# Optimization experiments

Hardware: AMD Instinct MI355X
Metric: run time of the kernel (lower is better)

The kernel has to match this reference:

```python
import jax, jax.numpy as jnp
import numpy as np

EPS = 1e-12


def _phi(e):
    # e: [C, L] -> pairwise euclidean distances [C, C], diagonal zeroed
    sq = jnp.sum(e * e, axis=1)                      # [C]
    prod = e @ e.T                                   # [C, C]
    d2 = sq[:, None] + sq[None, :] - 2.0 * prod
    d = jnp.sqrt(jnp.clip(d2, EPS, None))
    C = e.shape[0]
    return d * (1.0 - jnp.eye(C, dtype=e.dtype))


def setup_inputs() -> dict:
    key = jax.random.key(0)
    k1, k2, k3 = jax.random.split(key, 3)
    N, C, L = 64, 512, 256
    le_student = jax.random.normal(k1, (N, C, L), dtype=jnp.float32)
    le_teacher = jax.random.normal(k2, (N, C, L), dtype=jnp.float32)
    targets = jax.random.randint(k3, (N, C), 0, 2, dtype=jnp.int32)
    return {"le_student": le_student, "le_teacher": le_teacher, "targets": targets}


def reference(le_student, le_teacher, targets):
    N, C, L = le_student.shape
    m = targets.astype(le_student.dtype)             # [N, C] 0/1 mask
    es = le_student * m[:, :, None]                  # zero out negative rows
    et = le_teacher * m[:, :, None]

    Ds = jax.vmap(_phi)(es)                          # [N, C, C]
    Dt = jax.vmap(_phi)(et)                          # [N, C, C]

    eye = jnp.eye(C, dtype=m.dtype)
    pm = m[:, :, None] * m[:, None, :]               # pairs of positive rows
    offdiag = pm * (1.0 - eye)                       # off-diagonal positive pairs

    npos = jnp.sum(m, axis=1)                        # [N]
    cnt = npos * (npos - 1.0)                        # entries with d > 0 in submatrix
    valid = npos > 1.0
    safe_cnt = jnp.maximum(cnt, 1.0)

    mean_s = jnp.sum(Ds * offdiag, axis=(1, 2)) / safe_cnt
    mean_t = jax.lax.stop_gradient(jnp.sum(Dt * offdiag, axis=(1, 2)) / safe_cnt)
    mean_s = jnp.where(valid, mean_s, 1.0)
    mean_t = jnp.where(valid, mean_t, 1.0)

    d = Ds / mean_s[:, None, None]
    td = jax.lax.stop_gradient(Dt / mean_t[:, None, None])

    diff = d - td
    adiff = jnp.abs(diff)
    huber = jnp.where(adiff < 1.0, 0.5 * diff * diff, adiff - 0.5)

    per = jnp.sum(huber * pm, axis=(1, 2)) / jnp.maximum(npos, 1.0)
    return jnp.sum(jnp.where(valid, per, 0.0))
```

## Files before the change

kernel.cpp:

```cpp
#include <hip/hip_runtime.h>
#include <hip/hip_bf16.h>
#include <hip/hip_fp16.h>
#include <math.h>

#define NB 64
#define CC 512
#define LL 256

typedef __attribute__((ext_vector_type(4))) float floatx4;
typedef __attribute__((ext_vector_type(8))) short short8;

static __device__ __forceinline__ unsigned f2bf2(float x, float y) {
    __hip_bfloat162 h = __float22bfloat162_rn(make_float2(x, y));
    union { __hip_bfloat162 h; unsigned u; } c; c.h = h;
    return c.u;
}
static __device__ __forceinline__ unsigned short f2h(float x) {
    __half h = __float2half_rn(x);
    union { __half h; unsigned short u; } c; c.h = h;
    return c.u;
}
static __device__ __forceinline__ float h2f(unsigned u) {
    union { unsigned short u; __half h; } c; c.u = (unsigned short)u;
    return __half2float(c.h);
}

static __device__ __forceinline__ bool decode_tile(int t, int u, int& tI, int& tJ) {
    if (t >= (u * (u + 1)) >> 1) return false;
    tI = 0;
    while (t >= u - tI) { t -= u - tI; ++tI; }
    tJ = tI + t;
    return true;
}

__global__ __launch_bounds__(256) void dist_kernel(
    const float* __restrict__ S, const float* __restrict__ T,
    const int* __restrict__ targets,
    float* __restrict__ sumS, float* __restrict__ sumT,
    unsigned short* __restrict__ Ds, unsigned short* __restrict__ Dt,
    float* __restrict__ out)
{
    const int bx = blockIdx.x;
    const int n = bx & (NB - 1);
    const int q = bx >> 6;
    const int mat = q & 1, t = q >> 1;
    const int tid = threadIdx.x;
    const int w = tid >> 6, lane = tid & 63;

    __shared__ __align__(16) unsigned short lds[2][2][64][40];
    __shared__ float s_norm[2][64];
    __shared__ float red[4];
    __shared__ int s_idx[CC];
    __shared__ int s_cnt[8], s_off[8];
    __shared__ int s_np;

    if (bx == 0 && tid == 0) out[0] = 0.0f;

    const int* tg = targets + n * CC;
    const bool p0 = tg[tid] != 0;
    const bool p1 = tg[tid + 256] != 0;
    const unsigned long long m0 = __ballot(p0);
    const unsigned long long m1 = __ballot(p1);
    if (lane == 0) { s_cnt[w] = __popcll(m0); s_cnt[4 + w] = __popcll(m1); }
    __syncthreads();
    if (tid == 0) {
        int a = 0;
        for (int i = 0; i < 8; ++i) { s_off[i] = a; a += s_cnt[i]; }
        s_np = a;
    }
    __syncthreads();
    const unsigned long long below = (1ull << lane) - 1ull;
    if (p0) s_idx[s_off[w] + __popcll(m0 & below)] = tid;
    if (p1) s_idx[s_off[4 + w] + __popcll(m1 & below)] = tid + 256;
    const int np = s_np;
    __syncthreads();

    if (np < 2) return;
    int tI, tJ;
    if (!decode_tile(t, (np + 63) >> 6, tI, tJ)) return;
    const bool diag = (tI == tJ);

    const float* P = (mat ? T : S) + (size_t)n * CC * LL;
    unsigned short* Dout = (mat ? Dt : Ds) + (((size_t)t * NB + n) << 12);

    const int srow = w * 32 + (lane >> 1);
    const int half = lane & 1;
    const bool stager = diag ? (srow < 64) : true;
    const int ab = srow >> 6, rloc = srow & 63;
    const int gk = (ab ? tJ : tI) * 64 + rloc;
    const int row = s_idx[(gk < np) ? gk : 0];
    const char* rp = (const char*)P + (size_t)row * (LL * 4) + half * 64;

    float4 pre[4];
    float nsum = 0.0f;
    if (stager) {
        #pragma unroll
        for (int i = 0; i < 4; ++i) pre[i] = *(const float4*)(rp + i * 16);
    }

    const int m16 = lane & 15, quad = lane >> 4;
    const int bufB = diag ? 0 : 1;
    const int wrow = w * 16;

    floatx4 acc[4];
    #pragma unroll
    for (int c = 0; c < 4; ++c) { acc[c][0] = 0; acc[c][1] = 0; acc[c][2] = 0; acc[c][3] = 0; }

    for (int kk = 0; kk < 8; ++kk) {
        const int pb = kk & 1;
        if (stager) {
            #pragma unroll
            for (int i = 0; i < 4; ++i)
                nsum += pre[i].x * pre[i].x + pre[i].y * pre[i].y +
                        pre[i].z * pre[i].z + pre[i].w * pre[i].w;
            unsigned short* dst = &lds[ab][pb][rloc][half * 16];
            *(uint2*)(dst + 0)  = make_uint2(f2bf2(pre[0].x, pre[0].y), f2bf2(pre[0].z, pre[0].w));
            *(uint2*)(dst + 4)  = make_uint2(f2bf2(pre[1].x, pre[1].y), f2bf2(pre[1].z, pre[1].w));
            *(uint2*)(dst + 8)  = make_uint2(f2bf2(pre[2].x, pre[2].y), f2bf2(pre[2].z, pre[2].w));
            *(uint2*)(dst + 12) = make_uint2(f2bf2(pre[3].x, pre[3].y), f2bf2(pre[3].z, pre[3].w));
        }
        __syncthreads();
        if (stager && kk < 7) {
            #pragma unroll
            for (int i = 0; i < 4; ++i)
                pre[i] = *(const float4*)(rp + (kk + 1) * 128 + i * 16);
        }
        const short8 a = *(const short8*)&lds[0][pb][wrow + m16][quad * 8];
        #pragma unroll
        for (int c = 0; c < 4; ++c) {
            const short8 b = *(const short8*)&lds[bufB][pb][c * 16 + m16][quad * 8];
            acc[c] = __builtin_amdgcn_mfma_f32_16x16x32_bf16(a, b, acc[c], 0, 0, 0);
        }
    }

    if (stager) {
        const float v = nsum + __shfl_xor(nsum, 1);
        if (half == 0) s_norm[ab][rloc] = v;
    }
    __syncthreads();

    float l0 = 0.0f;
    #pragma unroll
    for (int c = 0; c < 4; ++c) {
        const int colL = c * 16 + m16;
        const int gj = tJ * 64 + colL;
        const float nB = s_norm[bufB][colL];
        #pragma unroll
        for (int r = 0; r < 4; ++r) {
            const int rowL = wrow + quad * 4 + r;
            const int gi = tI * 64 + rowL;
            const float d = sqrtf(fmaxf(s_norm[0][rowL] + nB - 2.0f * acc[c][r], 1e-12f));
            if (gi < np && gj < np && gi != gj) l0 += d;
            Dout[rowL * 64 + colL] = f2h(d);
        }
    }

    #pragma unroll
    for (int o = 32; o; o >>= 1) l0 += __shfl_down(l0, o);
    if (lane == 0) red[w] = l0;
    __syncthreads();
    if (tid == 0) {
        const float wgt = diag ? 1.0f : 2.0f;
        (mat ? sumT : sumS)[t * NB + n] = wgt * (red[0] + red[1] + red[2] + red[3]);
    }
}

__global__ __launch_bounds__(256) void huber_kernel(
    const int* __restrict__ targets,
    const float* __restrict__ sumS, const float* __restrict__ sumT,
    const unsigned short* __restrict__ Ds, const unsigned short* __restrict__ Dt,
    float* __restrict__ out)
{
    const int bx = blockIdx.x;
    const int n = bx & (NB - 1), t = bx >> 6;
    const int tid = threadIdx.x;
    const int w = tid >> 6, lane = tid & 63;

    __shared__ int s_cnt[8];
    __shared__ float red[4];

    const int* tg = targets + n * CC;
    const unsigned long long m0 = __ballot(tg[tid] != 0);
    const unsigned long long m1 = __ballot(tg[tid + 256] != 0);
    if (lane == 0) { s_cnt[w] = __popcll(m0); s_cnt[4 + w] = __popcll(m1); }
    __syncthreads();
    int np = 0;
    #pragma unroll
    for (int i = 0; i < 8; ++i) np += s_cnt[i];

    if (np < 2) return;
    const int u = (np + 63) >> 6;
    int tI, tJ;
    if (!decode_tile(t, u, tI, tJ)) return;
    const int ntiles = (u * (u + 1)) >> 1;

    float a = 0.0f, b = 0.0f;
    if (lane < ntiles) { a = sumS[lane * NB + n]; b = sumT[lane * NB + n]; }
    #pragma unroll
    for (int o = 32; o; o >>= 1) { a += __shfl_down(a, o); b += __shfl_down(b, o); }
    a = __shfl(a, 0); b = __shfl(b, 0);

    const float cnt = (float)np * (float)(np - 1);
    const float inv_ms = cnt / a;
    const float inv_mt = cnt / b;

    const size_t slot = ((size_t)t * NB + n) << 12;
    const uint4* ps = (const uint4*)(Ds + slot);
    const uint4* pt = (const uint4*)(Dt + slot);

    float h = 0.0f;
    #pragma unroll
    for (int it = 0; it < 2; ++it) {
        const int g = it * 256 + tid;
        const uint4 va = ps[g];
        const uint4 vb = pt[g];
        const unsigned aw[4] = { va.x, va.y, va.z, va.w };
        const unsigned bw[4] = { vb.x, vb.y, vb.z, vb.w };
        const int e0 = g * 8;
        #pragma unroll
        for (int k = 0; k < 8; ++k) {
            const int e = e0 + k;
            const int gi = tI * 64 + (e >> 6);
            const int gj = tJ * 64 + (e & 63);
            if (gi < np && gj < np && gi != gj) {
                const unsigned wa = aw[k >> 1], wb = bw[k >> 1];
                const float ds = h2f((k & 1) ? (wa >> 16) : (wa & 0xffffu));
                const float dt = h2f((k & 1) ? (wb >> 16) : (wb & 0xffffu));
                const float diff = ds * inv_ms - dt * inv_mt;
                const float ad = fabsf(diff);
                h += (ad < 1.0f) ? 0.5f * diff * diff : ad - 0.5f;
            }
        }
    }

    #pragma unroll
    for (int o = 32; o; o >>= 1) h += __shfl_down(h, o);
    if (lane == 0) red[w] = h;
    __syncthreads();
    if (tid == 0) {
        const float wgt = (tI == tJ) ? 1.0f : 2.0f;
        atomicAdd(out, wgt * (red[0] + red[1] + red[2] + red[3]) / (float)np);
    }
}

extern "C" void kernel_launch(void* const* d_in, const int* in_sizes, int n_in,
                              void* d_out, int out_size, void* d_ws, size_t ws_size,
                              hipStream_t stream) {
    const float* S = (const float*)d_in[0];
    const float* T = (const float*)d_in[1];
    const int* targets = (const int*)d_in[2];
    float* out = (float*)d_out;

    char* p = (char*)d_ws;
    float* sumS = (float*)p;   p += (size_t)36 * NB * 4;
    float* sumT = (float*)p;   p += (size_t)36 * NB * 4;
    p = (char*)(((size_t)p + 255) & ~(size_t)255);
    unsigned short* Ds = (unsigned short*)p;   p += (size_t)36 * NB * 4096 * 2;
    unsigned short* Dt = (unsigned short*)p;

    dist_kernel<<<72 * NB, 256, 0, stream>>>(S, T, targets, sumS, sumT, Ds, Dt, out);
    huber_kernel<<<36 * NB, 256, 0, stream>>>(targets, sumS, sumT, Ds, Dt, out);
}
```

Before: 122.2 us.

## Add pack kernel that compacts positive rows to bf16 with precomputed norms

```diff
diff --git a/kernel.cpp b/kernel.cpp
--- a/kernel.cpp
+++ b/kernel.cpp
@@ -33,28 +33,23 @@
     return true;
 }
 
-__global__ __launch_bounds__(256) void dist_kernel(
+__global__ __launch_bounds__(256) void pack_kernel(
     const float* __restrict__ S, const float* __restrict__ T,
     const int* __restrict__ targets,
-    float* __restrict__ sumS, float* __restrict__ sumT,
-    unsigned short* __restrict__ Ds, unsigned short* __restrict__ Dt,
+    int* __restrict__ npos, float* __restrict__ norms,
+    unsigned short* __restrict__ Sc, unsigned short* __restrict__ Tc,
     float* __restrict__ out)
 {
     const int bx = blockIdx.x;
     const int n = bx & (NB - 1);
     const int q = bx >> 6;
-    const int mat = q & 1, t = q >> 1;
+    const int mat = q & 1, slice = q >> 1;
     const int tid = threadIdx.x;
     const int w = tid >> 6, lane = tid & 63;
 
-    __shared__ __align__(16) unsigned short lds[2][2][64][40];
-    __shared__ float s_norm[2][64];
-    __shared__ float red[4];
     __shared__ int s_idx[CC];
     __shared__ int s_cnt[8], s_off[8];
     __shared__ int s_np;
-
-    if (bx == 0 && tid == 0) out[0] = 0.0f;
 
     const int* tg = targets + n * CC;
     const bool p0 = tg[tid] != 0;
@@ -67,6 +62,8 @@
         int a = 0;
         for (int i = 0; i < 8; ++i) { s_off[i] = a; a += s_cnt[i]; }
         s_np = a;
+        if (mat == 0 && slice == 0) npos[n] = a;
+        if (bx == 0) out[0] = 0.0f;
     }
     __syncthreads();
     const unsigned long long below = (1ull << lane) - 1ull;
@@ -75,28 +72,77 @@
     const int np = s_np;
     __syncthreads();
 
+    const int r = slice * 32 + (tid >> 3);
+    const int sub = tid & 7;
+    if (r >= np) return;
+    const int src = s_idx[r];
+    const float* P = (mat ? T : S) + ((size_t)n * CC + src) * LL + sub * 32;
+    unsigned short* Q = (mat ? Tc : Sc) + ((size_t)n * CC + r) * LL + sub * 32;
+
+    float4 v[8];
+    #pragma unroll
+    for (int i = 0; i < 8; ++i) v[i] = *(const float4*)(P + i * 4);
+    float ns = 0.0f;
+    #pragma unroll
+    for (int i = 0; i < 8; ++i)
+        ns += v[i].x * v[i].x + v[i].y * v[i].y + v[i].z * v[i].z + v[i].w * v[i].w;
+    ns += __shfl_xor(ns, 1); ns += __shfl_xor(ns, 2); ns += __shfl_xor(ns, 4);
+    if (sub == 0) norms[((size_t)mat * NB + n) * CC + r] = ns;
+
+    uint2 o[8];
+    #pragma unroll
+    for (int i = 0; i < 8; ++i) o[i] = make_uint2(f2bf2(v[i].x, v[i].y), f2bf2(v[i].z, v[i].w));
+    *(uint4*)(Q + 0)  = make_uint4(o[0].x, o[0].y, o[1].x, o[1].y);
+    *(uint4*)(Q + 8)  = make_uint4(o[2].x, o[2].y, o[3].x, o[3].y);
+    *(uint4*)(Q + 16) = make_uint4(o[4].x, o[4].y, o[5].x, o[5].y);
+    *(uint4*)(Q + 24) = make_uint4(o[6].x, o[6].y, o[7].x, o[7].y);
+}
+
+__global__ __launch_bounds__(256) void dist_kernel(
+    const unsigned short* __restrict__ Sc, const unsigned short* __restrict__ Tc,
+    const int* __restrict__ npos, const float* __restrict__ norms,
+    float* __restrict__ sumS, float* __restrict__ sumT,
+    unsigned short* __restrict__ Ds, unsigned short* __restrict__ Dt)
+{
+    const int bx = blockIdx.x;
+    const int n = bx & (NB - 1);
+    const int q = bx >> 6;
+    const int mat = q & 1, t = q >> 1;
+    const int np = npos[n];
     if (np < 2) return;
     int tI, tJ;
     if (!decode_tile(t, (np + 63) >> 6, tI, tJ)) return;
     const bool diag = (tI == tJ);
 
-    const float* P = (mat ? T : S) + (size_t)n * CC * LL;
+    __shared__ __align__(16) unsigned short lds[2][2][64][40];
+    __shared__ float s_norm[2][64];
+    __shared__ float red[4];
+
+    const int tid = threadIdx.x;
+    const int w = tid >> 6, lane = tid & 63;
+
+    const unsigned short* Pc = (mat ? Tc : Sc) + (size_t)n * CC * LL;
+    const float* nr = norms + ((size_t)mat * NB + n) * CC;
     unsigned short* Dout = (mat ? Dt : Ds) + (((size_t)t * NB + n) << 12);
+
+    if (tid < 128) {
+        const int abn = tid >> 6, rn = tid & 63;
+        if (!diag || abn == 0) {
+            const int g = (abn ? tJ : tI) * 64 + rn;
+            s_norm[abn][rn] = nr[(g < np) ? g : (np - 1)];
+        }
+    }
 
     const int srow = w * 32 + (lane >> 1);
     const int half = lane & 1;
     const bool stager = diag ? (srow < 64) : true;
     const int ab = srow >> 6, rloc = srow & 63;
     const int gk = (ab ? tJ : tI) * 64 + rloc;
-    const int row = s_idx[(gk < np) ? gk : 0];
-    const char* rp = (const char*)P + (size_t)row * (LL * 4) + half * 64;
-
-    float4 pre[4];
-    float nsum = 0.0f;
-    if (stager) {
-        #pragma unroll
-        for (int i = 0; i < 4; ++i) pre[i] = *(const float4*)(rp + i * 16);
-    }
+    const int crow = (gk < np) ? gk : (np - 1);
+    const unsigned char* rp = (const unsigned char*)(Pc + (size_t)crow * LL) + half * 32;
+
+    uint4 pre0, pre1;
+    if (stager) { pre0 = *(const uint4*)rp; pre1 = *(const uint4*)(rp + 16); }
 
     const int m16 = lane & 15, quad = lane >> 4;
     const int bufB = diag ? 0 : 1;
@@ -109,21 +155,14 @@
     for (int kk = 0; kk < 8; ++kk) {
         const int pb = kk & 1;
         if (stager) {
-            #pragma unroll
-            for (int i = 0; i < 4; ++i)
-                nsum += pre[i].x * pre[i].x + pre[i].y * pre[i].y +
-                        pre[i].z * pre[i].z + pre[i].w * pre[i].w;
             unsigned short* dst = &lds[ab][pb][rloc][half * 16];
-            *(uint2*)(dst + 0)  = make_uint2(f2bf2(pre[0].x, pre[0].y), f2bf2(pre[0].z, pre[0].w));
-            *(uint2*)(dst + 4)  = make_uint2(f2bf2(pre[1].x, pre[1].y), f2bf2(pre[1].z, pre[1].w));
-            *(uint2*)(dst + 8)  = make_uint2(f2bf2(pre[2].x, pre[2].y), f2bf2(pre[2].z, pre[2].w));
-            *(uint2*)(dst + 12) = make_uint2(f2bf2(pre[3].x, pre[3].y), f2bf2(pre[3].z, pre[3].w));
+            *(uint4*)(dst + 0) = pre0;
+            *(uint4*)(dst + 8) = pre1;
         }
         __syncthreads();
         if (stager && kk < 7) {
-            #pragma unroll
-            for (int i = 0; i < 4; ++i)
-                pre[i] = *(const float4*)(rp + (kk + 1) * 128 + i * 16);
+            pre0 = *(const uint4*)(rp + (kk + 1) * 64);
+            pre1 = *(const uint4*)(rp + (kk + 1) * 64 + 16);
         }
         const short8 a = *(const short8*)&lds[0][pb][wrow + m16][quad * 8];
         #pragma unroll
@@ -132,12 +171,6 @@
             acc[c] = __builtin_amdgcn_mfma_f32_16x16x32_bf16(a, b, acc[c], 0, 0, 0);
         }
     }
-
-    if (stager) {
-        const float v = nsum + __shfl_xor(nsum, 1);
-        if (half == 0) s_norm[ab][rloc] = v;
-    }
-    __syncthreads();
 
     float l0 = 0.0f;
     #pragma unroll
@@ -166,33 +199,23 @@
 }
 
 __global__ __launch_bounds__(256) void huber_kernel(
-    const int* __restrict__ targets,
+    const int* __restrict__ npos,
     const float* __restrict__ sumS, const float* __restrict__ sumT,
     const unsigned short* __restrict__ Ds, const unsigned short* __restrict__ Dt,
     float* __restrict__ out)
 {
     const int bx = blockIdx.x;
     const int n = bx & (NB - 1), t = bx >> 6;
-    const int tid = threadIdx.x;
-    const int w = tid >> 6, lane = tid & 63;
-
-    __shared__ int s_cnt[8];
-    __shared__ float red[4];
-
-    const int* tg = targets + n * CC;
-    const unsigned long long m0 = __ballot(tg[tid] != 0);
-    const unsigned long long m1 = __ballot(tg[tid + 256] != 0);
-    if (lane == 0) { s_cnt[w] = __popcll(m0); s_cnt[4 + w] = __popcll(m1); }
-    __syncthreads();
-    int np = 0;
-    #pragma unroll
-    for (int i = 0; i < 8; ++i) np += s_cnt[i];
-
+    const int np = npos[n];
     if (np < 2) return;
     const int u = (np + 63) >> 6;
     int tI, tJ;
     if (!decode_tile(t, u, tI, tJ)) return;
     const int ntiles = (u * (u + 1)) >> 1;
+
+    const int tid = threadIdx.x;
+    const int w = tid >> 6, lane = tid & 63;
+    __shared__ float red[4];
 
     float a = 0.0f, b = 0.0f;
     if (lane < ntiles) { a = sumS[lane * NB + n]; b = sumT[lane * NB + n]; }
@@ -252,12 +275,17 @@
     float* out = (float*)d_out;
 
     char* p = (char*)d_ws;
+    int* npos = (int*)p;       p += 256;
+    float* norms = (float*)p;  p += (size_t)2 * NB * CC * 4;
     float* sumS = (float*)p;   p += (size_t)36 * NB * 4;
     float* sumT = (float*)p;   p += (size_t)36 * NB * 4;
     p = (char*)(((size_t)p + 255) & ~(size_t)255);
-    unsigned short* Ds = (unsigned short*)p;   p += (size_t)36 * NB * 4096 * 2;
+    unsigned short* Sc = (unsigned short*)p;  p += (size_t)NB * CC * LL * 2;
+    unsigned short* Tc = (unsigned short*)p;  p += (size_t)NB * CC * LL * 2;
+    unsigned short* Ds = (unsigned short*)p;  p += (size_t)36 * NB * 4096 * 2;
     unsigned short* Dt = (unsigned short*)p;
 
-    dist_kernel<<<72 * NB, 256, 0, stream>>>(S, T, targets, sumS, sumT, Ds, Dt, out);
-    huber_kernel<<<36 * NB, 256, 0, stream>>>(targets, sumS, sumT, Ds, Dt, out);
-}
+    pack_kernel<<<32 * NB, 256, 0, stream>>>(S, T, targets, npos, norms, Sc, Tc, out);
+    dist_kernel<<<72 * NB, 256, 0, stream>>>(Sc, Tc, npos, norms, sumS, sumT, Ds, Dt);
+    huber_kernel<<<36 * NB, 256, 0, stream>>>(npos, sumS, sumT, Ds, Dt, out);
+}
```

Measured after the change: 129.2 us. 1.06x slower.

## Fuse distance and Huber kernels using last-block-done atomic counters

Applied to the files above, without the earlier changes.

```diff
diff --git a/kernel.cpp b/kernel.cpp
--- a/kernel.cpp
+++ b/kernel.cpp
@@ -23,6 +23,12 @@
 static __device__ __forceinline__ float h2f(unsigned u) {
     union { unsigned short u; __half h; } c; c.u = (unsigned short)u;
     return __half2float(c.h);
+}
+static __device__ __forceinline__ float ld_agent_f32(const float* p) {
+    return __hip_atomic_load(p, __ATOMIC_RELAXED, __HIP_MEMORY_SCOPE_AGENT);
+}
+static __device__ __forceinline__ unsigned long long ld_agent_u64(const unsigned long long* p) {
+    return __hip_atomic_load(p, __ATOMIC_RELAXED, __HIP_MEMORY_SCOPE_AGENT);
 }
 
 static __device__ __forceinline__ bool decode_tile(int t, int u, int& tI, int& tJ) {
@@ -33,9 +39,10 @@
     return true;
 }
 
-__global__ __launch_bounds__(256) void dist_kernel(
+__global__ __launch_bounds__(256) void mega_kernel(
     const float* __restrict__ S, const float* __restrict__ T,
     const int* __restrict__ targets,
+    int* __restrict__ bcnt, int* __restrict__ gcnt, float* __restrict__ hout,
     float* __restrict__ sumS, float* __restrict__ sumT,
     unsigned short* __restrict__ Ds, unsigned short* __restrict__ Dt,
     float* __restrict__ out)
@@ -52,9 +59,7 @@
     __shared__ float red[4];
     __shared__ int s_idx[CC];
     __shared__ int s_cnt[8], s_off[8];
-    __shared__ int s_np;
-
-    if (bx == 0 && tid == 0) out[0] = 0.0f;
+    __shared__ int s_np, s_flag;
 
     const int* tg = targets + n * CC;
     const bool p0 = tg[tid] != 0;
@@ -69,15 +74,38 @@
         s_np = a;
     }
     __syncthreads();
+    const int np = s_np;
+
+    if (np < 2) {
+        if (t != 0 || mat != 0) return;
+        if (tid == 0) {
+            hout[n] = 0.0f;
+            __threadfence();
+            s_flag = __hip_atomic_fetch_add(gcnt, 1, __ATOMIC_ACQ_REL, __HIP_MEMORY_SCOPE_AGENT);
+        }
+        __syncthreads();
+        if (s_flag == NB - 1) {
+            if (tid < 64) {
+                float v = ld_agent_f32(hout + tid);
+                #pragma unroll
+                for (int o = 32; o; o >>= 1) v += __shfl_down(v, o);
+                if (tid == 0) out[0] = v;
+            }
+        }
+        return;
+    }
+
+    const int u = (np + 63) >> 6;
+    const int ntiles = (u * (u + 1)) >> 1;
+    if (t >= ntiles) return;
+
     const unsigned long long below = (1ull << lane) - 1ull;
     if (p0) s_idx[s_off[w] + __popcll(m0 & below)] = tid;
     if (p1) s_idx[s_off[4 + w] + __popcll(m1 & below)] = tid + 256;
-    const int np = s_np;
-    __syncthreads();
-
-    if (np < 2) return;
+    __syncthreads();
+
     int tI, tJ;
-    if (!decode_tile(t, (np + 63) >> 6, tI, tJ)) return;
+    decode_tile(t, u, tI, tJ);
     const bool diag = (tI == tJ);
 
     const float* P = (mat ? T : S) + (size_t)n * CC * LL;
@@ -162,40 +190,17 @@
     if (tid == 0) {
         const float wgt = diag ? 1.0f : 2.0f;
         (mat ? sumT : sumS)[t * NB + n] = wgt * (red[0] + red[1] + red[2] + red[3]);
-    }
-}
-
-__global__ __launch_bounds__(256) void huber_kernel(
-    const int* __restrict__ targets,
-    const float* __restrict__ sumS, const float* __restrict__ sumT,
-    const unsigned short* __restrict__ Ds, const unsigned short* __restrict__ Dt,
-    float* __restrict__ out)
-{
-    const int bx = blockIdx.x;
-    const int n = bx & (NB - 1), t = bx >> 6;
-    const int tid = threadIdx.x;
-    const int w = tid >> 6, lane = tid & 63;
-
-    __shared__ int s_cnt[8];
-    __shared__ float red[4];
-
-    const int* tg = targets + n * CC;
-    const unsigned long long m0 = __ballot(tg[tid] != 0);
-    const unsigned long long m1 = __ballot(tg[tid + 256] != 0);
-    if (lane == 0) { s_cnt[w] = __popcll(m0); s_cnt[4 + w] = __popcll(m1); }
-    __syncthreads();
-    int np = 0;
-    #pragma unroll
-    for (int i = 0; i < 8; ++i) np += s_cnt[i];
-
-    if (np < 2) return;
-    const int u = (np + 63) >> 6;
-    int tI, tJ;
-    if (!decode_tile(t, u, tI, tJ)) return;
-    const int ntiles = (u * (u + 1)) >> 1;
+        __threadfence();
+        s_flag = __hip_atomic_fetch_add(&bcnt[n], 1, __ATOMIC_ACQ_REL, __HIP_MEMORY_SCOPE_AGENT);
+    }
+    __syncthreads();
+    if (s_flag != 2 * ntiles - 1) return;
 
     float a = 0.0f, b = 0.0f;
-    if (lane < ntiles) { a = sumS[lane * NB + n]; b = sumT[lane * NB + n]; }
+    if (lane < ntiles) {
+        a = ld_agent_f32(&sumS[lane * NB + n]);
+        b = ld_agent_f32(&sumT[lane * NB + n]);
+    }
     #pragma unroll
     for (int o = 32; o; o >>= 1) { a += __shfl_down(a, o); b += __shfl_down(b, o); }
     a = __shfl(a, 0); b = __shfl(b, 0);
@@ -204,33 +209,35 @@
     const float inv_ms = cnt / a;
     const float inv_mt = cnt / b;
 
-    const size_t slot = ((size_t)t * NB + n) << 12;
-    const uint4* ps = (const uint4*)(Ds + slot);
-    const uint4* pt = (const uint4*)(Dt + slot);
-
     float h = 0.0f;
-    #pragma unroll
-    for (int it = 0; it < 2; ++it) {
-        const int g = it * 256 + tid;
-        const uint4 va = ps[g];
-        const uint4 vb = pt[g];
-        const unsigned aw[4] = { va.x, va.y, va.z, va.w };
-        const unsigned bw[4] = { vb.x, vb.y, vb.z, vb.w };
-        const int e0 = g * 8;
-        #pragma unroll
-        for (int k = 0; k < 8; ++k) {
-            const int e = e0 + k;
-            const int gi = tI * 64 + (e >> 6);
-            const int gj = tJ * 64 + (e & 63);
-            if (gi < np && gj < np && gi != gj) {
-                const unsigned wa = aw[k >> 1], wb = bw[k >> 1];
-                const float ds = h2f((k & 1) ? (wa >> 16) : (wa & 0xffffu));
-                const float dt = h2f((k & 1) ? (wb >> 16) : (wb & 0xffffu));
-                const float diff = ds * inv_ms - dt * inv_mt;
-                const float ad = fabsf(diff);
-                h += (ad < 1.0f) ? 0.5f * diff * diff : ad - 0.5f;
+    for (int tt = 0; tt < ntiles; ++tt) {
+        int eI, eJ; decode_tile(tt, u, eI, eJ);
+        const float wgt = (eI == eJ) ? 1.0f : 2.0f;
+        const size_t slot = ((size_t)tt * NB + n) << 12;
+        const unsigned long long* ps = (const unsigned long long*)(Ds + slot);
+        const unsigned long long* pt = (const unsigned long long*)(Dt + slot);
+        float hl = 0.0f;
+        #pragma unroll
+        for (int it = 0; it < 4; ++it) {
+            const int g = it * 256 + tid;
+            const unsigned long long ua = ld_agent_u64(ps + g);
+            const unsigned long long ub = ld_agent_u64(pt + g);
+            const int e0 = g * 4;
+            #pragma unroll
+            for (int k = 0; k < 4; ++k) {
+                const int e = e0 + k;
+                const int gi = eI * 64 + (e >> 6);
+                const int gj = eJ * 64 + (e & 63);
+                if (gi < np && gj < np && gi != gj) {
+                    const float ds = h2f((unsigned)((ua >> (16 * k)) & 0xffffu));
+                    const float dt = h2f((unsigned)((ub >> (16 * k)) & 0xffffu));
+                    const float diff = ds * inv_ms - dt * inv_mt;
+                    const float ad = fabsf(diff);
+                    hl += (ad < 1.0f) ? 0.5f * diff * diff : ad - 0.5f;
+                }
             }
         }
+        h += wgt * hl;
     }
 
     #pragma unroll
@@ -238,8 +245,18 @@
     if (lane == 0) red[w] = h;
     __syncthreads();
     if (tid == 0) {
-        const float wgt = (tI == tJ) ? 1.0f : 2.0f;
-        atomicAdd(out, wgt * (red[0] + red[1] + red[2] + red[3]) / (float)np);
+        hout[n] = (red[0] + red[1] + red[2] + red[3]) / (float)np;
+        __threadfence();
+        s_flag = __hip_atomic_fetch_add(gcnt, 1, __ATOMIC_ACQ_REL, __HIP_MEMORY_SCOPE_AGENT);
+    }
+    __syncthreads();
+    if (s_flag == NB - 1) {
+        if (tid < 64) {
+            float v = ld_agent_f32(hout + tid);
+            #pragma unroll
+            for (int o = 32; o; o >>= 1) v += __shfl_down(v, o);
+            if (tid == 0) out[0] = v;
+        }
     }
 }
 
@@ -252,12 +269,17 @@
     float* out = (float*)d_out;
 
     char* p = (char*)d_ws;
-    float* sumS = (float*)p;   p += (size_t)36 * NB * 4;
-    float* sumT = (float*)p;   p += (size_t)36 * NB * 4;
+    int* bcnt = (int*)p;
+    int* gcnt = (int*)(p + 256);
+    float* hout = (float*)(p + 512);
+    float* sumS = (float*)(p + 768);
+    float* sumT = sumS + 36 * NB;
+    p += 768 + (size_t)2 * 36 * NB * 4;
     p = (char*)(((size_t)p + 255) & ~(size_t)255);
-    unsigned short* Ds = (unsigned short*)p;   p += (size_t)36 * NB * 4096 * 2;
+    unsigned short* Ds = (unsigned short*)p;  p += (size_t)36 * NB * 4096 * 2;
     unsigned short* Dt = (unsigned short*)p;
 
-    dist_kernel<<<72 * NB, 256, 0, stream>>>(S, T, targets, sumS, sumT, Ds, Dt, out);
-    huber_kernel<<<36 * NB, 256, 0, stream>>>(targets, sumS, sumT, Ds, Dt, out);
-}
+    hipMemsetAsync(bcnt, 0, 512, stream);
+    mega_kernel<<<72 * NB, 256, 0, stream>>>(S, T, targets, bcnt, gcnt, hout,
+                                             sumS, sumT, Ds, Dt, out);
+}
```

Result: slower. 246.7 us (+101.9%).

## Enlarge distance-kernel tiles to 128x128 with 512-thread blocks

Applied to the files above, without the earlier changes.

```diff
diff --git a/kernel.cpp b/kernel.cpp
--- a/kernel.cpp
+++ b/kernel.cpp
@@ -33,7 +33,7 @@
     return true;
 }
 
-__global__ __launch_bounds__(256) void dist_kernel(
+__global__ __launch_bounds__(512) void dist_kernel(
     const float* __restrict__ S, const float* __restrict__ T,
     const int* __restrict__ targets,
     float* __restrict__ sumS, float* __restrict__ sumT,
@@ -43,13 +43,13 @@
     const int bx = blockIdx.x;
     const int n = bx & (NB - 1);
     const int q = bx >> 6;
-    const int mat = q & 1, t = q >> 1;
+    const int mat = q & 1, t2 = q >> 1;
     const int tid = threadIdx.x;
     const int w = tid >> 6, lane = tid & 63;
 
-    __shared__ __align__(16) unsigned short lds[2][2][64][40];
-    __shared__ float s_norm[2][64];
-    __shared__ float red[4];
+    __shared__ __align__(16) unsigned short lds[2][2][128][40];
+    __shared__ float s_norm[2][128];
+    __shared__ float red[8];
     __shared__ int s_idx[CC];
     __shared__ int s_cnt[8], s_off[8];
     __shared__ int s_np;
@@ -58,10 +58,8 @@
 
     const int* tg = targets + n * CC;
     const bool p0 = tg[tid] != 0;
-    const bool p1 = tg[tid + 256] != 0;
     const unsigned long long m0 = __ballot(p0);
-    const unsigned long long m1 = __ballot(p1);
-    if (lane == 0) { s_cnt[w] = __popcll(m0); s_cnt[4 + w] = __popcll(m1); }
+    if (lane == 0) s_cnt[w] = __popcll(m0);
     __syncthreads();
     if (tid == 0) {
         int a = 0;
@@ -69,25 +67,25 @@
         s_np = a;
     }
     __syncthreads();
+    const int np = s_np;
+    if (np < 2) return;
+    const int u2 = (np + 127) >> 7;
+    int tI2, tJ2;
+    if (!decode_tile(t2, u2, tI2, tJ2)) return;
+    const bool diag = (tI2 == tJ2);
+
     const unsigned long long below = (1ull << lane) - 1ull;
     if (p0) s_idx[s_off[w] + __popcll(m0 & below)] = tid;
-    if (p1) s_idx[s_off[4 + w] + __popcll(m1 & below)] = tid + 256;
-    const int np = s_np;
-    __syncthreads();
-
-    if (np < 2) return;
-    int tI, tJ;
-    if (!decode_tile(t, (np + 63) >> 6, tI, tJ)) return;
-    const bool diag = (tI == tJ);
+    __syncthreads();
 
     const float* P = (mat ? T : S) + (size_t)n * CC * LL;
-    unsigned short* Dout = (mat ? Dt : Ds) + (((size_t)t * NB + n) << 12);
-
-    const int srow = w * 32 + (lane >> 1);
-    const int half = lane & 1;
-    const bool stager = diag ? (srow < 64) : true;
-    const int ab = srow >> 6, rloc = srow & 63;
-    const int gk = (ab ? tJ : tI) * 64 + rloc;
+    unsigned short* Dout = (mat ? Dt : Ds) + (size_t)(t2 * NB + n) * 16384;
+
+    const int srow = tid >> 1;
+    const int half = tid & 1;
+    const bool stager = diag ? (srow < 128) : true;
+    const int ab = srow >> 7, rloc = srow & 127;
+    const int gk = (ab ? tJ2 : tI2) * 128 + rloc;
     const int row = s_idx[(gk < np) ? gk : 0];
     const char* rp = (const char*)P + (size_t)row * (LL * 4) + half * 64;
 
@@ -102,9 +100,9 @@
     const int bufB = diag ? 0 : 1;
     const int wrow = w * 16;
 
-    floatx4 acc[4];
-    #pragma unroll
-    for (int c = 0; c < 4; ++c) { acc[c][0] = 0; acc[c][1] = 0; acc[c][2] = 0; acc[c][3] = 0; }
+    floatx4 acc[8];
+    #pragma unroll
+    for (int c = 0; c < 8; ++c) { acc[c][0] = 0; acc[c][1] = 0; acc[c][2] = 0; acc[c][3] = 0; }
 
     for (int kk = 0; kk < 8; ++kk) {
         const int pb = kk & 1;
@@ -127,7 +125,7 @@
         }
         const short8 a = *(const short8*)&lds[0][pb][wrow + m16][quad * 8];
         #pragma unroll
-        for (int c = 0; c < 4; ++c) {
+        for (int c = 0; c < 8; ++c) {
             const short8 b = *(const short8*)&lds[bufB][pb][c * 16 + m16][quad * 8];
             acc[c] = __builtin_amdgcn_mfma_f32_16x16x32_bf16(a, b, acc[c], 0, 0, 0);
         }
@@ -141,17 +139,17 @@
 
     float l0 = 0.0f;
     #pragma unroll
-    for (int c = 0; c < 4; ++c) {
+    for (int c = 0; c < 8; ++c) {
         const int colL = c * 16 + m16;
-        const int gj = tJ * 64 + colL;
+        const int gj = tJ2 * 128 + colL;
         const float nB = s_norm[bufB][colL];
         #pragma unroll
         for (int r = 0; r < 4; ++r) {
             const int rowL = wrow + quad * 4 + r;
-            const int gi = tI * 64 + rowL;
+            const int gi = tI2 * 128 + rowL;
             const float d = sqrtf(fmaxf(s_norm[0][rowL] + nB - 2.0f * acc[c][r], 1e-12f));
             if (gi < np && gj < np && gi != gj) l0 += d;
-            Dout[rowL * 64 + colL] = f2h(d);
+            Dout[rowL * 128 + colL] = f2h(d);
         }
     }
 
@@ -161,7 +159,10 @@
     __syncthreads();
     if (tid == 0) {
         const float wgt = diag ? 1.0f : 2.0f;
-        (mat ? sumT : sumS)[t * NB + n] = wgt * (red[0] + red[1] + red[2] + red[3]);
+        float s = 0.0f;
+        #pragma unroll
+        for (int i = 0; i < 8; ++i) s += red[i];
+        (mat ? sumT : sumS)[t2 * NB + n] = wgt * s;
     }
 }
 
@@ -192,10 +193,12 @@
     const int u = (np + 63) >> 6;
     int tI, tJ;
     if (!decode_tile(t, u, tI, tJ)) return;
-    const int ntiles = (u * (u + 1)) >> 1;
+
+    const int u2 = (np + 127) >> 7;
+    const int ntiles2 = (u2 * (u2 + 1)) >> 1;
 
     float a = 0.0f, b = 0.0f;
-    if (lane < ntiles) { a = sumS[lane * NB + n]; b = sumT[lane * NB + n]; }
+    if (lane < ntiles2) { a = sumS[lane * NB + n]; b = sumT[lane * NB + n]; }
     #pragma unroll
     for (int o = 32; o; o >>= 1) { a += __shfl_down(a, o); b += __shfl_down(b, o); }
     a = __shfl(a, 0); b = __shfl(b, 0);
@@ -204,24 +207,26 @@
     const float inv_ms = cnt / a;
     const float inv_mt = cnt / b;
 
-    const size_t slot = ((size_t)t * NB + n) << 12;
-    const uint4* ps = (const uint4*)(Ds + slot);
-    const uint4* pt = (const uint4*)(Dt + slot);
+    const int I2 = tI >> 1, J2 = tJ >> 1;
+    const int t2 = I2 * u2 - ((I2 * (I2 - 1)) >> 1) + (J2 - I2);
+    const int rBase = (tI & 1) * 64, cBase = (tJ & 1) * 64;
+    const size_t base = (size_t)(t2 * NB + n) * 16384 + (size_t)rBase * 128 + cBase;
 
     float h = 0.0f;
     #pragma unroll
     for (int it = 0; it < 2; ++it) {
         const int g = it * 256 + tid;
-        const uint4 va = ps[g];
-        const uint4 vb = pt[g];
+        const int e0 = g * 8;
+        const int r64 = e0 >> 6, c64 = e0 & 63;
+        const size_t addr = base + (size_t)r64 * 128 + c64;
+        const uint4 va = *(const uint4*)(Ds + addr);
+        const uint4 vb = *(const uint4*)(Dt + addr);
         const unsigned aw[4] = { va.x, va.y, va.z, va.w };
         const unsigned bw[4] = { vb.x, vb.y, vb.z, vb.w };
-        const int e0 = g * 8;
+        const int gi = tI * 64 + r64;
         #pragma unroll
         for (int k = 0; k < 8; ++k) {
-            const int e = e0 + k;
-            const int gi = tI * 64 + (e >> 6);
-            const int gj = tJ * 64 + (e & 63);
+            const int gj = tJ * 64 + c64 + k;
             if (gi < np && gj < np && gi != gj) {
                 const unsigned wa = aw[k >> 1], wb = bw[k >> 1];
                 const float ds = h2f((k & 1) ? (wa >> 16) : (wa & 0xffffu));
@@ -252,12 +257,12 @@
     float* out = (float*)d_out;
 
     char* p = (char*)d_ws;
-    float* sumS = (float*)p;   p += (size_t)36 * NB * 4;
-    float* sumT = (float*)p;   p += (size_t)36 * NB * 4;
+    float* sumS = (float*)p;   p += (size_t)10 * NB * 4;
+    float* sumT = (float*)p;   p += (size_t)10 * NB * 4;
     p = (char*)(((size_t)p + 255) & ~(size_t)255);
-    unsigned short* Ds = (unsigned short*)p;   p += (size_t)36 * NB * 4096 * 2;
+    unsigned short* Ds = (unsigned short*)p;  p += (size_t)10 * NB * 16384 * 2;
     unsigned short* Dt = (unsigned short*)p;
 
-    dist_kernel<<<72 * NB, 256, 0, stream>>>(S, T, targets, sumS, sumT, Ds, Dt, out);
+    dist_kernel<<<20 * NB, 512, 0, stream>>>(S, T, targets, sumS, sumT, Ds, Dt, out);
     huber_kernel<<<36 * NB, 256, 0, stream>>>(targets, sumS, sumT, Ds, Dt, out);
 }
```

Measured after the change: 128.6 us. +5.2%, slower.
